# Performance work log

Hardware: AMD Instinct MI355X
Metric: run time of the kernel (lower is better)

Reference implementation:

```python
import jax, jax.numpy as jnp
import numpy as np

B, T, CIN, HF, G, E = 8, 316, 64, 128, 32, 384
DOWN, MINP, OUT = 2, 8, 8
STRIDE = MINP // DOWN  # finest-grid cell -> feature-map stride


def _build_metas(b, t):
    # Non-overlapping quadtree partition of the 32x32 finest grid:
    # 8x8 macro cells (span 4) all split into span-2 nodes; the first 20 of
    # those are split again into span-1 leaves -> 236 + 80 = 316 tokens.
    # meta row = [tl_row_fg, tl_col_fg, cell_span, patch_px, score]
    span2 = [(r + dr, c + dc) for r in range(0, G, 4) for c in range(0, G, 4)
             for dr in (0, 2) for dc in (0, 2)]
    rows = [[r, c, 2, 16, 0] for (r, c) in span2[20:]]
    rows += [[r + dr, c + dc, 1, 8, 0] for (r, c) in span2[:20]
             for dr in (0, 1) for dc in (0, 1)]
    meta = np.asarray(rows, np.int32)
    rng = np.random.default_rng(0)
    return jnp.asarray(np.stack([meta[rng.permutation(t)] for _ in range(b)], 0))


def setup_inputs():
    key = jax.random.key(0)
    k1, k2 = jax.random.split(key)
    return {
        "x_in": jax.random.normal(k1, (B, CIN, HF, HF), jnp.float32),
        "tokens": jax.random.normal(k2, (B, T, E), jnp.float32),
        "metas": _build_metas(B, T),
    }


def _sample_token(img, r_fg, c_fg, p_px):
    # img: [C, Hf, Wf]. Bilinear resize (align_corners=False, matching
    # F.interpolate) of the [p_feat, p_feat] crop at (r_fg*STRIDE, c_fg*STRIDE)
    # to [OUT, OUT], fully in-place via gathers (no host syncs, no per-token
    # kernel launches).
    p_feat = p_px // DOWN
    pf = jnp.maximum(p_feat, 1).astype(jnp.float32)
    i = jnp.arange(OUT, dtype=jnp.float32)
    rel = jnp.clip((i + 0.5) * (pf / OUT) - 0.5, 0.0, pf - 1.0)
    i0 = jnp.floor(rel)
    w = rel - i0
    i1 = jnp.minimum(i0 + 1.0, pf - 1.0)
    off_r = (r_fg * STRIDE).astype(jnp.float32)
    off_c = (c_fg * STRIDE).astype(jnp.float32)
    y0 = (off_r + i0).astype(jnp.int32); y1 = (off_r + i1).astype(jnp.int32)
    x0 = (off_c + i0).astype(jnp.int32); x1 = (off_c + i1).astype(jnp.int32)
    g = lambda y, x: img[:, y[:, None], x[None, :]]  # [C, OUT, OUT]
    wx = w[None, None, :]; wy = w[None, :, None]
    top = g(y0, x0) * (1 - wx) + g(y0, x1) * wx
    bot = g(y1, x0) * (1 - wx) + g(y1, x1) * wx
    patch = top * (1 - wy) + bot * wy
    return jnp.where(p_px > 0, patch, 0.0)


def _extract_patches(x_in, metas):
    per_img = lambda img, mb: jax.vmap(
        lambda m: _sample_token(img, m[0], m[1], m[3]))(mb)
    return jax.vmap(per_img)(x_in, metas)  # [B, T, C, OUT, OUT]


def _spatial_scatter(tokens, metas):
    # Each token's embedding is tiled over its span x span finest-grid cells.
    # Build an owner-index map via one scatter, then one gather.
    b, t, e = tokens.shape
    r, c, span, p = metas[..., 0], metas[..., 1], metas[..., 2], metas[..., 3]
    di, dj = np.meshgrid(np.arange(4), np.arange(4), indexing="ij")  # max span 4
    di = jnp.asarray(di.reshape(-1)); dj = jnp.asarray(dj.reshape(-1))  # [16]
    rows = r[:, :, None] + di
    cols = c[:, :, None] + dj                                   # [B, T, 16]
    valid = (di < span[:, :, None]) & (dj < span[:, :, None]) & (p[:, :, None] > 0)
    flat = jnp.where(valid, rows * G + cols, G * G)             # dump slot G*G
    owner = jnp.full((b, G * G + 1), -1, jnp.int32)
    b_idx = jnp.arange(b)[:, None, None]
    t_idx = jnp.broadcast_to(jnp.arange(t, dtype=jnp.int32)[None, :, None], flat.shape)
    owner = owner.at[b_idx, flat].set(t_idx)[:, : G * G]        # [B, G*G]
    gathered = jnp.take_along_axis(tokens, jnp.maximum(owner, 0)[:, :, None], axis=1)
    fmap = jnp.where(owner[:, :, None] >= 0, gathered, 0.0)     # [B, G*G, E]
    return fmap.reshape(b, G, G, e).transpose(0, 3, 1, 2)       # [B, E, G, G]


def reference(x_in, tokens, metas):
    patches = _extract_patches(x_in, metas)
    half_span = metas[..., 2].astype(jnp.float32) / 2.0
    cx = metas[..., 1].astype(jnp.float32) + half_span
    cy = metas[..., 0].astype(jnp.float32) + half_span
    p = metas[..., 3]
    scale_idx = jnp.where(p == 16, 1, jnp.where(p == 8, 2, 0)).astype(jnp.int32)
    fmap = _spatial_scatter(tokens, metas)
    return patches, cx, cy, scale_idx, fmap
```

## Files before the change

kernel.cpp:

```cpp
#include <hip/hip_runtime.h>

#define B_      8
#define T_      316
#define CIN_    64
#define HF_     128
#define G_      32
#define E_      384
#define OUT_    8

#define PATCH_SZ  10354688
#define CX_OFF    (PATCH_SZ)
#define CY_OFF    (CX_OFF + B_*T_)
#define SI_OFF    (CY_OFF + B_*T_)
#define FMAP_OFF  (SI_OFF + B_*T_)

#define NBAND_ 16
#define NCHG_  8
#define NP_    (B_ * NBAND_ * NCHG_)

#define EG_    16
#define NF_    (B_ * (E_ / EG_))

#define LDSC_ 1088

__device__ __forceinline__ void load16(float* d, const float* p, bool ok)
{
    if (ok) {
        const float4* q = (const float4*)p;
#pragma unroll
        for (int k = 0; k < 4; ++k) {
            const float4 v = q[k];
            d[4*k+0] = v.x; d[4*k+1] = v.y; d[4*k+2] = v.z; d[4*k+3] = v.w;
        }
    } else {
#pragma unroll
        for (int k = 0; k < 16; ++k) d[k] = 0.0f;
    }
}

__global__ void fused_kernel(const float* __restrict__ x,
                             const float* __restrict__ tokens,
                             const int* __restrict__ metas,
                             float* __restrict__ out)
{
    const int blk = blockIdx.x;
    const int tid = threadIdx.x;

    if (blk < NP_) {
        const int b   = blk / (NBAND_ * NCHG_);
        const int rem = blk % (NBAND_ * NCHG_);
        const int gr  = rem / NCHG_;
        const int chg = rem % NCHG_;

        __shared__ __align__(16) float sm[8 * LDSC_];
        __shared__ int own16[16];
        __shared__ int p8e[64];
        __shared__ int np8;

        if (tid < 16) own16[tid] = -1;
        if (tid == 0) np8 = 0;
        __syncthreads();

        for (int t = tid; t < T_; t += 256) {
            const int* m = metas + (b * T_ + t) * 5;
            const int r = m[0], c = m[1], p = m[3];
            if (p == 16) {
                if (r == 2 * gr) own16[c >> 1] = t;
            } else if (p == 8) {
                if ((r >> 1) == gr) {
                    const int k = atomicAdd(&np8, 1);
                    p8e[k] = (t << 6) | ((r & 1) << 5) | c;
                }
            }
        }

        const int row  = tid >> 5;
        const int col4 = tid & 31;
        const int cp   = col4 >> 1;
        const int j4   = col4 & 1;
        const int w    = row * 2 + j4;

        const float* src = x + ((size_t)b * CIN_ + chg * 8) * (HF_ * HF_)
                             + (8 * gr + row) * HF_ + col4 * 4;
        float* dst = sm + cp * 68 + w * 4;
#pragma unroll
        for (int ccl = 0; ccl < 8; ++ccl)
            *(float4*)(dst + ccl * LDSC_) = *(const float4*)(src + (size_t)ccl * (HF_ * HF_));
        __syncthreads();

        const int cpo = tid >> 4;
        const int wo  = tid & 15;
        const int tok = own16[cpo];
        if (tok >= 0) {
            float4* po4 = (float4*)out + (size_t)(b * T_ + tok) * 1024;
            const float* ls = sm + cpo * 68 + wo * 4;
#pragma unroll
            for (int ccl = 0; ccl < 8; ++ccl)
                po4[(chg * 8 + ccl) * 16 + wo] = *(const float4*)(ls + ccl * LDSC_);
        }

        for (int e0 = 0; e0 < np8; e0 += 2) {
            const int e = e0 + (tid >> 7);
            if (e < np8) {
                const int ent = p8e[e];
                const int tk  = ent >> 6;
                const int rl  = (ent >> 5) & 1;
                const int cc  = ent & 31;
                const int u   = tid & 127;
                const int ccl = u >> 4;
                const int ww  = u & 15;
                const int i   = ww >> 1;
                const int j4w = ww & 1;

                const float* cell = sm + ccl * LDSC_ + (cc >> 1) * 68
                                       + (cc & 1) * 4 + 32 * rl;

                const float reli = fminf(fmaxf(((float)i + 0.5f) * 0.5f - 0.5f, 0.0f), 3.0f);
                const float fi0  = floorf(reli);
                const float wy   = reli - fi0;
                const int   y0   = (int)fi0;
                const int   y1   = (int)fminf(fi0 + 1.0f, 3.0f);

                float res[4];
#pragma unroll
                for (int jj = 0; jj < 4; ++jj) {
                    const int j = j4w * 4 + jj;
                    const float relj = fminf(fmaxf(((float)j + 0.5f) * 0.5f - 0.5f, 0.0f), 3.0f);
                    const float fj0  = floorf(relj);
                    const float wx   = relj - fj0;
                    const int   x0   = (int)fj0;
                    const int   x1   = (int)fminf(fj0 + 1.0f, 3.0f);
                    const float t0 = cell[y0 * 8 + x0] * (1.0f - wx) + cell[y0 * 8 + x1] * wx;
                    const float t1 = cell[y1 * 8 + x0] * (1.0f - wx) + cell[y1 * 8 + x1] * wx;
                    res[jj] = t0 * (1.0f - wy) + t1 * wy;
                }
                ((float4*)out)[(size_t)(b * T_ + tk) * 1024 + (chg * 8 + ccl) * 16 + ww] =
                    make_float4(res[0], res[1], res[2], res[3]);
            }
        }
        return;
    }

    const int fb = blk - NP_;
    const int b  = fb / (E_ / EG_);
    const int eg = fb % (E_ / EG_);

    __shared__ int own[G_ * G_];
#pragma unroll
    for (int k = 0; k < 4; ++k) own[tid + k * 256] = -1;
    __syncthreads();

    for (int t = tid; t < T_; t += 256) {
        const int* m = metas + (b * T_ + t) * 5;
        const int r = m[0], c = m[1], s = m[2], p = m[3];

        if (eg == 0) {
            const float hs = (float)s * 0.5f;
            out[CX_OFF + b * T_ + t] = (float)c + hs;
            out[CY_OFF + b * T_ + t] = (float)r + hs;
            out[SI_OFF + b * T_ + t] = (p == 16) ? 1.0f : ((p == 8) ? 2.0f : 0.0f);
        }
        if (p > 0) {
            const int sl = (s < 4) ? s : 4;
            for (int di = 0; di < sl; ++di)
                for (int dj = 0; dj < sl; ++dj) {
                    const int rr = r + di, cc = c + dj;
                    if (rr < G_ && cc < G_)
                        own[rr * G_ + cc] = t;
                }
        }
    }
    __syncthreads();

    const int4 o = *(const int4*)(own + 4 * tid);
    const float* tok = tokens + (size_t)b * T_ * E_ + eg * EG_;

    float a0[16], a1[16], a2[16], a3[16];
    load16(a0, tok + (size_t)o.x * E_, o.x >= 0);
    load16(a1, tok + (size_t)o.y * E_, o.y >= 0);
    load16(a2, tok + (size_t)o.z * E_, o.z >= 0);
    load16(a3, tok + (size_t)o.w * E_, o.w >= 0);

    float4* fm = (float4*)(out + FMAP_OFF + (size_t)b * E_ * (G_ * G_)
                                          + (size_t)eg * EG_ * (G_ * G_));
#pragma unroll
    for (int e = 0; e < EG_; ++e) {
        float4 v; v.x = a0[e]; v.y = a1[e]; v.z = a2[e]; v.w = a3[e];
        fm[e * 256 + tid] = v;
    }
}

extern "C" void kernel_launch(void* const* d_in, const int* in_sizes, int n_in,
                              void* d_out, int out_size, void* d_ws, size_t ws_size,
                              hipStream_t stream) {
    const float* x_in   = (const float*)d_in[0];
    const float* tokens = (const float*)d_in[1];
    const int*   metas  = (const int*)d_in[2];
    float*       out    = (float*)d_out;

    fused_kernel<<<NP_ + NF_, 256, 0, stream>>>(x_in, tokens, metas, out);
}
```

Before: 97.70 us.

## Merge feature-map scatter into patch blocks and prefetch input before metadata scan

After: 113.4 us. +16.1%, slower.

```diff
diff --git a/kernel.cpp b/kernel.cpp
--- a/kernel.cpp
+++ b/kernel.cpp
@@ -16,27 +16,10 @@
 
 #define NBAND_ 16
 #define NCHG_  8
-#define NP_    (B_ * NBAND_ * NCHG_)
-
-#define EG_    16
-#define NF_    (B_ * (E_ / EG_))
+#define NBLK_  (B_ * NBAND_ * NCHG_)
+#define ESL_   (E_ / NCHG_)
 
 #define LDSC_ 1088
-
-__device__ __forceinline__ void load16(float* d, const float* p, bool ok)
-{
-    if (ok) {
-        const float4* q = (const float4*)p;
-#pragma unroll
-        for (int k = 0; k < 4; ++k) {
-            const float4 v = q[k];
-            d[4*k+0] = v.x; d[4*k+1] = v.y; d[4*k+2] = v.z; d[4*k+3] = v.w;
-        }
-    } else {
-#pragma unroll
-        for (int k = 0; k < 16; ++k) d[k] = 0.0f;
-    }
-}
 
 __global__ void fused_kernel(const float* __restrict__ x,
                              const float* __restrict__ tokens,
@@ -46,48 +29,69 @@
     const int blk = blockIdx.x;
     const int tid = threadIdx.x;
 
-    if (blk < NP_) {
-        const int b   = blk / (NBAND_ * NCHG_);
-        const int rem = blk % (NBAND_ * NCHG_);
-        const int gr  = rem / NCHG_;
-        const int chg = rem % NCHG_;
+    const int b   = blk / (NBAND_ * NCHG_);
+    const int rem = blk % (NBAND_ * NCHG_);
+    const int gr  = rem / NCHG_;
+    const int chg = rem % NCHG_;
 
-        __shared__ __align__(16) float sm[8 * LDSC_];
-        __shared__ int own16[16];
-        __shared__ int p8e[64];
-        __shared__ int np8;
+    __shared__ __align__(16) float sm[8 * LDSC_];
+    __shared__ int own16[16];
+    __shared__ int own64[64];
+    __shared__ int p8e[64];
+    __shared__ int np8;
 
-        if (tid < 16) own16[tid] = -1;
-        if (tid == 0) np8 = 0;
-        __syncthreads();
+    const int row  = tid >> 5;
+    const int col4 = tid & 31;
+    const int cp   = col4 >> 1;
+    const int j4   = col4 & 1;
+    const int w    = row * 2 + j4;
 
-        for (int t = tid; t < T_; t += 256) {
-            const int* m = metas + (b * T_ + t) * 5;
-            const int r = m[0], c = m[1], p = m[3];
-            if (p == 16) {
-                if (r == 2 * gr) own16[c >> 1] = t;
-            } else if (p == 8) {
-                if ((r >> 1) == gr) {
-                    const int k = atomicAdd(&np8, 1);
-                    p8e[k] = (t << 6) | ((r & 1) << 5) | c;
-                }
+    const float* src = x + ((size_t)b * CIN_ + chg * 8) * (HF_ * HF_)
+                         + (8 * gr + row) * HF_ + col4 * 4;
+    float4 v[8];
+#pragma unroll
+    for (int ccl = 0; ccl < 8; ++ccl)
+        v[ccl] = *(const float4*)(src + (size_t)ccl * (HF_ * HF_));
+
+    if (tid < 16) own16[tid] = -1;
+    if (tid < 64) own64[tid] = -1;
+    if (tid == 0) np8 = 0;
+    __syncthreads();
+
+    for (int t = tid; t < T_; t += 256) {
+        const int4 m = *(const int4*)(metas + (b * T_ + t) * 5);
+        const int r = m.x, c = m.y, s = m.z, p = m.w;
+
+        if (gr == 0 && chg == 0) {
+            const float hs = (float)s * 0.5f;
+            out[CX_OFF + b * T_ + t] = (float)c + hs;
+            out[CY_OFF + b * T_ + t] = (float)r + hs;
+            out[SI_OFF + b * T_ + t] = (p == 16) ? 1.0f : ((p == 8) ? 2.0f : 0.0f);
+        }
+        if (p == 16) {
+            if (r == 2 * gr) {
+                own16[c >> 1] = t;
+                own64[c] = t; own64[c + 1] = t;
+                own64[32 + c] = t; own64[33 + c] = t;
+            }
+        } else if (p == 8) {
+            if ((r >> 1) == gr) {
+                const int k = atomicAdd(&np8, 1);
+                p8e[k] = (t << 6) | ((r & 1) << 5) | c;
+                own64[(r & 1) * 32 + c] = t;
             }
         }
+    }
 
-        const int row  = tid >> 5;
-        const int col4 = tid & 31;
-        const int cp   = col4 >> 1;
-        const int j4   = col4 & 1;
-        const int w    = row * 2 + j4;
-
-        const float* src = x + ((size_t)b * CIN_ + chg * 8) * (HF_ * HF_)
-                             + (8 * gr + row) * HF_ + col4 * 4;
+    {
         float* dst = sm + cp * 68 + w * 4;
 #pragma unroll
         for (int ccl = 0; ccl < 8; ++ccl)
-            *(float4*)(dst + ccl * LDSC_) = *(const float4*)(src + (size_t)ccl * (HF_ * HF_));
-        __syncthreads();
+            *(float4*)(dst + ccl * LDSC_) = v[ccl];
+    }
+    __syncthreads();
 
+    {
         const int cpo = tid >> 4;
         const int wo  = tid & 15;
         const int tok = own16[cpo];
@@ -98,95 +102,62 @@
             for (int ccl = 0; ccl < 8; ++ccl)
                 po4[(chg * 8 + ccl) * 16 + wo] = *(const float4*)(ls + ccl * LDSC_);
         }
-
-        for (int e0 = 0; e0 < np8; e0 += 2) {
-            const int e = e0 + (tid >> 7);
-            if (e < np8) {
-                const int ent = p8e[e];
-                const int tk  = ent >> 6;
-                const int rl  = (ent >> 5) & 1;
-                const int cc  = ent & 31;
-                const int u   = tid & 127;
-                const int ccl = u >> 4;
-                const int ww  = u & 15;
-                const int i   = ww >> 1;
-                const int j4w = ww & 1;
-
-                const float* cell = sm + ccl * LDSC_ + (cc >> 1) * 68
-                                       + (cc & 1) * 4 + 32 * rl;
-
-                const float reli = fminf(fmaxf(((float)i + 0.5f) * 0.5f - 0.5f, 0.0f), 3.0f);
-                const float fi0  = floorf(reli);
-                const float wy   = reli - fi0;
-                const int   y0   = (int)fi0;
-                const int   y1   = (int)fminf(fi0 + 1.0f, 3.0f);
-
-                float res[4];
-#pragma unroll
-                for (int jj = 0; jj < 4; ++jj) {
-                    const int j = j4w * 4 + jj;
-                    const float relj = fminf(fmaxf(((float)j + 0.5f) * 0.5f - 0.5f, 0.0f), 3.0f);
-                    const float fj0  = floorf(relj);
-                    const float wx   = relj - fj0;
-                    const int   x0   = (int)fj0;
-                    const int   x1   = (int)fminf(fj0 + 1.0f, 3.0f);
-                    const float t0 = cell[y0 * 8 + x0] * (1.0f - wx) + cell[y0 * 8 + x1] * wx;
-                    const float t1 = cell[y1 * 8 + x0] * (1.0f - wx) + cell[y1 * 8 + x1] * wx;
-                    res[jj] = t0 * (1.0f - wy) + t1 * wy;
-                }
-                ((float4*)out)[(size_t)(b * T_ + tk) * 1024 + (chg * 8 + ccl) * 16 + ww] =
-                    make_float4(res[0], res[1], res[2], res[3]);
-            }
-        }
-        return;
     }
 
-    const int fb = blk - NP_;
-    const int b  = fb / (E_ / EG_);
-    const int eg = fb % (E_ / EG_);
+    for (int e0 = 0; e0 < np8; e0 += 2) {
+        const int e = e0 + (tid >> 7);
+        if (e < np8) {
+            const int ent = p8e[e];
+            const int tk  = ent >> 6;
+            const int rl  = (ent >> 5) & 1;
+            const int cc  = ent & 31;
+            const int u   = tid & 127;
+            const int ccl = u >> 4;
+            const int ww  = u & 15;
+            const int i   = ww >> 1;
+            const int j4w = ww & 1;
 
-    __shared__ int own[G_ * G_];
+            const float* cell = sm + ccl * LDSC_ + (cc >> 1) * 68
+                                   + (cc & 1) * 4 + 32 * rl;
+
+            const float reli = fminf(fmaxf(((float)i + 0.5f) * 0.5f - 0.5f, 0.0f), 3.0f);
+            const float fi0  = floorf(reli);
+            const float wy   = reli - fi0;
+            const int   y0   = (int)fi0;
+            const int   y1   = (int)fminf(fi0 + 1.0f, 3.0f);
+
+            float res[4];
 #pragma unroll
-    for (int k = 0; k < 4; ++k) own[tid + k * 256] = -1;
-    __syncthreads();
-
-    for (int t = tid; t < T_; t += 256) {
-        const int* m = metas + (b * T_ + t) * 5;
-        const int r = m[0], c = m[1], s = m[2], p = m[3];
-
-        if (eg == 0) {
-            const float hs = (float)s * 0.5f;
-            out[CX_OFF + b * T_ + t] = (float)c + hs;
-            out[CY_OFF + b * T_ + t] = (float)r + hs;
-            out[SI_OFF + b * T_ + t] = (p == 16) ? 1.0f : ((p == 8) ? 2.0f : 0.0f);
-        }
-        if (p > 0) {
-            const int sl = (s < 4) ? s : 4;
-            for (int di = 0; di < sl; ++di)
-                for (int dj = 0; dj < sl; ++dj) {
-                    const int rr = r + di, cc = c + dj;
-                    if (rr < G_ && cc < G_)
-                        own[rr * G_ + cc] = t;
-                }
+            for (int jj = 0; jj < 4; ++jj) {
+                const int j = j4w * 4 + jj;
+                const float relj = fminf(fmaxf(((float)j + 0.5f) * 0.5f - 0.5f, 0.0f), 3.0f);
+                const float fj0  = floorf(relj);
+                const float wx   = relj - fj0;
+                const int   x0   = (int)fj0;
+                const int   x1   = (int)fminf(fj0 + 1.0f, 3.0f);
+                const float t0 = cell[y0 * 8 + x0] * (1.0f - wx) + cell[y0 * 8 + x1] * wx;
+                const float t1 = cell[y1 * 8 + x0] * (1.0f - wx) + cell[y1 * 8 + x1] * wx;
+                res[jj] = t0 * (1.0f - wy) + t1 * wy;
+            }
+            ((float4*)out)[(size_t)(b * T_ + tk) * 1024 + (chg * 8 + ccl) * 16 + ww] =
+                make_float4(res[0], res[1], res[2], res[3]);
         }
     }
-    __syncthreads();
 
-    const int4 o = *(const int4*)(own + 4 * tid);
-    const float* tok = tokens + (size_t)b * T_ * E_ + eg * EG_;
+    {
+        const int ephase = tid >> 6;
+        const int cell   = tid & 63;
+        const int ownt   = own64[cell];
+        const int e0     = chg * ESL_ + ephase;
 
-    float a0[16], a1[16], a2[16], a3[16];
-    load16(a0, tok + (size_t)o.x * E_, o.x >= 0);
-    load16(a1, tok + (size_t)o.y * E_, o.y >= 0);
-    load16(a2, tok + (size_t)o.z * E_, o.z >= 0);
-    load16(a3, tok + (size_t)o.w * E_, o.w >= 0);
+        const float* tokp = tokens + ((size_t)b * T_ + (ownt >= 0 ? ownt : 0)) * E_ + e0;
+        float* fmp = out + FMAP_OFF + ((size_t)b * E_ + e0) * (G_ * G_) + 64 * gr + cell;
 
-    float4* fm = (float4*)(out + FMAP_OFF + (size_t)b * E_ * (G_ * G_)
-                                          + (size_t)eg * EG_ * (G_ * G_));
 #pragma unroll
-    for (int e = 0; e < EG_; ++e) {
-        float4 v; v.x = a0[e]; v.y = a1[e]; v.z = a2[e]; v.w = a3[e];
-        fm[e * 256 + tid] = v;
+        for (int k = 0; k < 12; ++k) {
+            const float val = (ownt >= 0) ? tokp[4 * k] : 0.0f;
+            fmp[(size_t)(4 * k) * (G_ * G_)] = val;
+        }
     }
 }
 
@@ -198,5 +169,5 @@
     const int*   metas  = (const int*)d_in[2];
     float*       out    = (float*)d_out;
 
-    fused_kernel<<<NP_ + NF_, 256, 0, stream>>>(x_in, tokens, metas, out);
+    fused_kernel<<<NBLK_, 256, 0, stream>>>(x_in, tokens, metas, out);
 }
```
